# Performance work log

Hardware: AMD Instinct MI355X
Metric: run time of the kernel (lower is better)

## Reference

```python
import jax, jax.numpy as jnp
import numpy as np

N = 131072          # batch_size(64) * cycle_size(2048) total graph nodes
E = 2097152         # N * avg_degree(16) edges


def _gcn_block(x, edge_index, W_self, W_nbr, b):
    """GraphConv-style STGCN spatial block: self-transform + mean-aggregated
    neighbor transform over edge_index (gather -> segment-reduce -> scatter)."""
    src, dst = edge_index[0], edge_index[1]
    msg = jax.ops.segment_sum(x[src], dst, num_segments=N)            # [N, C_in]
    deg = jax.ops.segment_sum(jnp.ones((edge_index.shape[1],), x.dtype), dst,
                              num_segments=N)                          # [N]
    agg = msg / jnp.maximum(deg, 1.0)[:, None]
    return x @ W_self + agg @ W_nbr + b


def setup_inputs() -> dict:
    key = jax.random.key(0)
    ks = jax.random.split(key, 16)

    def lin(k, fan_in, fan_out):
        return jax.random.normal(k, (fan_in, fan_out), jnp.float32) / np.sqrt(fan_in)

    x = jax.random.normal(ks[0], (N, 16), jnp.float32)
    edge_index = jax.random.randint(ks[1], (2, E), 0, N)
    batch = jnp.zeros((N,), jnp.int64) if jax.config.jax_enable_x64 else jnp.zeros((N,), jnp.int32)

    return {
        "x": x,
        "edge_index": edge_index,
        "batch": batch,
        "W_lin": lin(ks[2], 16, 16),
        "b_lin": jnp.zeros((16,), jnp.float32),
        # block3: 16 -> 32
        "Ws3": lin(ks[3], 16, 32), "Wn3": lin(ks[4], 16, 32), "b3": jnp.zeros((32,), jnp.float32),
        # block2: 32 -> 64
        "Ws2": lin(ks[5], 32, 64), "Wn2": lin(ks[6], 32, 64), "b2": jnp.zeros((64,), jnp.float32),
        # block1: 64 -> 128
        "Ws1": lin(ks[7], 64, 128), "Wn1": lin(ks[8], 64, 128), "b1": jnp.zeros((128,), jnp.float32),
    }


def reference(x, edge_index, batch, W_lin, b_lin,
              Ws3, Wn3, b3, Ws2, Wn2, b2, Ws1, Wn1, b1):
    h = x @ W_lin + b_lin                                   # Linear(16,16)
    h = jax.nn.relu(_gcn_block(h, edge_index, Ws3, Wn3, b3))   # 16 -> 32
    h = jax.nn.relu(_gcn_block(h, edge_index, Ws2, Wn2, b2))   # 32 -> 64
    h = jax.nn.sigmoid(_gcn_block(h, edge_index, Ws1, Wn1, b1))  # 64 -> 128
    return h
```

## Files before the change

kernel.cpp:

```cpp
#include <hip/hip_runtime.h>
#include <cmath>


typedef __attribute__((ext_vector_type(8))) _Float16 half8;
typedef __attribute__((ext_vector_type(4))) float floatx4;

#define NBUCKET 512
#define BUCKET_SHIFT 8

__global__ __launch_bounds__(256) void bucket_hist_kernel(
    const int* __restrict__ dst, int* __restrict__ bcnt, int E, int EPB, int nblk) {
    __shared__ int lh[NBUCKET];
    for (int i = threadIdx.x; i < NBUCKET; i += 256) lh[i] = 0;
    __syncthreads();
    int base = blockIdx.x * EPB;
    int end  = min(base + EPB, E);
    for (int i = base + threadIdx.x; i < end; i += 256)
        atomicAdd(&lh[dst[i] >> BUCKET_SHIFT], 1);
    __syncthreads();
    for (int i = threadIdx.x; i < NBUCKET; i += 256)
        bcnt[i * nblk + blockIdx.x] = lh[i];
}

__global__ void scan1_kernel(const int* __restrict__ in, int* __restrict__ out,
                             int* __restrict__ bsum) {
    __shared__ int s[256];
    int i = blockIdx.x * 256 + threadIdx.x;
    int v = in[i];
    s[threadIdx.x] = v;
    __syncthreads();
    for (int off = 1; off < 256; off <<= 1) {
        int t = (threadIdx.x >= off) ? s[threadIdx.x - off] : 0;
        __syncthreads();
        s[threadIdx.x] += t;
        __syncthreads();
    }
    out[i] = s[threadIdx.x] - v;
    if (threadIdx.x == 255) bsum[blockIdx.x] = s[255];
}

__global__ void scan2_kernel(int* __restrict__ bsum, int NB) {
    extern __shared__ int s2[];
    int v = (threadIdx.x < NB) ? bsum[threadIdx.x] : 0;
    s2[threadIdx.x] = v;
    __syncthreads();
    for (int off = 1; off < NB; off <<= 1) {
        int t = (threadIdx.x >= off) ? s2[threadIdx.x - off] : 0;
        __syncthreads();
        s2[threadIdx.x] += t;
        __syncthreads();
    }
    if (threadIdx.x < NB) bsum[threadIdx.x] = s2[threadIdx.x] - v;
}

__global__ void scan3_kernel(int* __restrict__ out, const int* __restrict__ bsum) {
    int i = blockIdx.x * 256 + threadIdx.x;
    out[i] += bsum[blockIdx.x];
}

__global__ __launch_bounds__(256) void partition_kernel(
    const int* __restrict__ src, const int* __restrict__ dst,
    const int* __restrict__ bofs, int* __restrict__ part,
    int E, int EPB, int nblk) {
    __shared__ int cur[NBUCKET];
    for (int i = threadIdx.x; i < NBUCKET; i += 256)
        cur[i] = bofs[i * nblk + blockIdx.x];
    __syncthreads();
    int base = blockIdx.x * EPB;
    int end  = min(base + EPB, E);
    for (int i = base + threadIdx.x; i < end; i += 256) {
        int d = dst[i];
        int p = atomicAdd(&cur[d >> BUCKET_SHIFT], 1);
        part[p] = (src[i] << 8) | (d & 255);
    }
}

__global__ __launch_bounds__(256) void local_csr_kernel(
    const int* __restrict__ bofs, const int* __restrict__ part,
    int* __restrict__ row_ptr, int* __restrict__ csr_src,
    int N, int E, int nblk) {
    __shared__ int cnt[256];
    __shared__ int offs[256];
    const int u      = blockIdx.x;
    const int node0  = u << BUCKET_SHIFT;
    const int bstart = bofs[(size_t)u * nblk];
    const int bend   = (u + 1 < gridDim.x) ? bofs[(size_t)(u + 1) * nblk] : E;

    cnt[threadIdx.x] = 0;
    __syncthreads();
    for (int i = bstart + threadIdx.x; i < bend; i += 256)
        atomicAdd(&cnt[part[i] & 255], 1);
    __syncthreads();

    int v = cnt[threadIdx.x];
    offs[threadIdx.x] = v;
    __syncthreads();
    for (int off = 1; off < 256; off <<= 1) {
        int t = (threadIdx.x >= off) ? offs[threadIdx.x - off] : 0;
        __syncthreads();
        offs[threadIdx.x] += t;
        __syncthreads();
    }
    int excl = offs[threadIdx.x] - v;
    int rbase = bstart + excl;
    if (node0 + threadIdx.x < N) row_ptr[node0 + threadIdx.x] = rbase;
    if (u == 0 && threadIdx.x == 0) row_ptr[N] = E;
    __syncthreads();
    cnt[threadIdx.x] = rbase;
    __syncthreads();
    for (int i = bstart + threadIdx.x; i < bend; i += 256) {
        int e = part[i];
        int p = atomicAdd(&cnt[e & 255], 1);
        csr_src[p] = e >> 8;
    }
}

__global__ void wt_all_kernel(
    const float* __restrict__ Ws1, const float* __restrict__ Wn1, _Float16* __restrict__ Wt1,
    const float* __restrict__ Ws2, const float* __restrict__ Wn2, _Float16* __restrict__ Wt2,
    const float* __restrict__ Ws3, const float* __restrict__ Wn3, _Float16* __restrict__ Wt3) {
    int idx = blockIdx.x * 256 + threadIdx.x;
    const float *Ws, *Wn; _Float16* Wt; int CI, NOUT;
    if (idx < 16384)        { Ws = Ws1; Wn = Wn1; Wt = Wt1; CI = 64; NOUT = 128; }
    else if (idx < 20480)   { idx -= 16384; Ws = Ws2; Wn = Wn2; Wt = Wt2; CI = 32; NOUT = 64; }
    else if (idx < 21504)   { idx -= 20480; Ws = Ws3; Wn = Wn3; Wt = Wt3; CI = 16; NOUT = 32; }
    else return;
    int K = 2 * CI;
    int n = idx / K, k = idx - n * K;
    float v = (k < CI) ? Ws[(size_t)k * NOUT + n] : Wn[(size_t)(k - CI) * NOUT + n];
    Wt[n * K + k] = (_Float16)v;
}

__global__ void lin16_kernel(const float* __restrict__ x, const float* __restrict__ W,
                             const float* __restrict__ b, _Float16* __restrict__ h, int N) {
    __shared__ float sW[256];
    __shared__ float sb[16];
    sW[threadIdx.x] = W[threadIdx.x];
    if (threadIdx.x < 16) sb[threadIdx.x] = b[threadIdx.x];
    __syncthreads();
    int n = blockIdx.x * blockDim.x + threadIdx.x;
    if (n >= N) return;
    const float4* xr = (const float4*)(x + (size_t)n * 16);
    float4 x0 = xr[0], x1 = xr[1], x2 = xr[2], x3 = xr[3];
    float xi[16] = {x0.x, x0.y, x0.z, x0.w, x1.x, x1.y, x1.z, x1.w,
                    x2.x, x2.y, x2.z, x2.w, x3.x, x3.y, x3.z, x3.w};
    float o[16];
#pragma unroll
    for (int j = 0; j < 16; j++) o[j] = sb[j];
#pragma unroll
    for (int k = 0; k < 16; k++) {
        float xv = xi[k];
#pragma unroll
        for (int j = 0; j < 16; j++) o[j] += xv * sW[k * 16 + j];
    }
    half8 h0v, h1v;
#pragma unroll
    for (int j = 0; j < 8; j++) { h0v[j] = (_Float16)o[j]; h1v[j] = (_Float16)o[j + 8]; }
    half8* hr = (half8*)(h + (size_t)n * 16);
    hr[0] = h0v;
    hr[1] = h1v;
}

template <int C>
__global__ __launch_bounds__(256) void gather_kernel(
    const int* __restrict__ row_ptr, const int* __restrict__ csr_src,
    const _Float16* __restrict__ h, _Float16* __restrict__ agg, int N) {
    constexpr int GP = C / 8;
    int t = blockIdx.x * blockDim.x + threadIdx.x;
    int total = N * GP;
    if (t >= total) return;
    int n = t / GP;
    int g = t - n * GP;
    const int beg = row_ptr[n];
    const int end = row_ptr[n + 1];
    const size_t goff = (size_t)g * 8;

    float a0[8], a1[8];
#pragma unroll
    for (int i = 0; i < 8; i++) { a0[i] = 0.f; a1[i] = 0.f; }

    int j = beg;
    for (; j + 8 <= end; j += 8) {
        int i0 = csr_src[j + 0], i1 = csr_src[j + 1], i2 = csr_src[j + 2], i3 = csr_src[j + 3];
        int i4 = csr_src[j + 4], i5 = csr_src[j + 5], i6 = csr_src[j + 6], i7 = csr_src[j + 7];
        half8 v0 = *(const half8*)(h + (size_t)i0 * C + goff);
        half8 v1 = *(const half8*)(h + (size_t)i1 * C + goff);
        half8 v2 = *(const half8*)(h + (size_t)i2 * C + goff);
        half8 v3 = *(const half8*)(h + (size_t)i3 * C + goff);
        half8 v4 = *(const half8*)(h + (size_t)i4 * C + goff);
        half8 v5 = *(const half8*)(h + (size_t)i5 * C + goff);
        half8 v6 = *(const half8*)(h + (size_t)i6 * C + goff);
        half8 v7 = *(const half8*)(h + (size_t)i7 * C + goff);
#pragma unroll
        for (int i = 0; i < 8; i++) {
            a0[i] += ((float)v0[i] + (float)v2[i]) + ((float)v4[i] + (float)v6[i]);
            a1[i] += ((float)v1[i] + (float)v3[i]) + ((float)v5[i] + (float)v7[i]);
        }
    }
    if (j < end) {
        const int last = end - 1;
        int i0 = csr_src[j];
        int i1 = csr_src[min(j + 1, last)];
        int i2 = csr_src[min(j + 2, last)];
        int i3 = csr_src[min(j + 3, last)];
        int i4 = csr_src[min(j + 4, last)];
        int i5 = csr_src[min(j + 5, last)];
        int i6 = csr_src[min(j + 6, last)];
        int i7 = csr_src[min(j + 7, last)];
        half8 v0 = *(const half8*)(h + (size_t)i0 * C + goff);
        half8 v1 = *(const half8*)(h + (size_t)i1 * C + goff);
        half8 v2 = *(const half8*)(h + (size_t)i2 * C + goff);
        half8 v3 = *(const half8*)(h + (size_t)i3 * C + goff);
        half8 v4 = *(const half8*)(h + (size_t)i4 * C + goff);
        half8 v5 = *(const half8*)(h + (size_t)i5 * C + goff);
        half8 v6 = *(const half8*)(h + (size_t)i6 * C + goff);
        half8 v7 = *(const half8*)(h + (size_t)i7 * C + goff);
        float w1 = (j + 1 < end) ? 1.f : 0.f;
        float w2 = (j + 2 < end) ? 1.f : 0.f;
        float w3 = (j + 3 < end) ? 1.f : 0.f;
        float w4 = (j + 4 < end) ? 1.f : 0.f;
        float w5 = (j + 5 < end) ? 1.f : 0.f;
        float w6 = (j + 6 < end) ? 1.f : 0.f;
        float w7 = (j + 7 < end) ? 1.f : 0.f;
#pragma unroll
        for (int i = 0; i < 8; i++) {
            a0[i] += ((float)v0[i] + w2 * (float)v2[i]) + (w4 * (float)v4[i] + w6 * (float)v6[i]);
            a1[i] += (w1 * (float)v1[i] + w3 * (float)v3[i]) + (w5 * (float)v5[i] + w7 * (float)v7[i]);
        }
    }

    float inv = 1.0f / fmaxf((float)(end - beg), 1.0f);
    half8 r;
#pragma unroll
    for (int i = 0; i < 8; i++) r[i] = (_Float16)((a0[i] + a1[i]) * inv);
    *(half8*)(agg + (size_t)n * C + goff) = r;
}

template <int CI, int NOUT, int ACT, bool OUT_F16>
__global__ __launch_bounds__(256) void mfma_gemm_kernel(
    const _Float16* __restrict__ hbuf, const _Float16* __restrict__ abuf,
    const _Float16* __restrict__ Wt,
    const float* __restrict__ bias, void* __restrict__ outp, int N)
{
    constexpr int K   = 2 * CI;
    constexpr int KS  = K / 32;
    constexpr int CT  = NOUT / 16;
    constexpr int LDW = K + 8;
    __shared__ _Float16 Bt[NOUT * LDW];

    const int tid = threadIdx.x;
    for (int idx = tid; idx < NOUT * (K / 8); idx += 256) {
        int n  = idx / (K / 8);
        int kq = idx - n * (K / 8);
        *(half8*)&Bt[n * LDW + kq * 8] = *(const half8*)(Wt + (size_t)n * K + kq * 8);
    }
    __syncthreads();

    const int wave = tid >> 6;
    const int lane = tid & 63;
    const int m    = lane & 15;
    const int quad = lane >> 4;
    const int row0 = blockIdx.x * 64 + wave * 16;
    const size_t row = (size_t)(row0 + m);

    floatx4 acc[CT];
#pragma unroll
    for (int c = 0; c < CT; c++) acc[c] = (floatx4){0.f, 0.f, 0.f, 0.f};

#pragma unroll
    for (int s = 0; s < KS; s++) {
        int k8 = s * 32 + quad * 8;
        const _Float16* Ap = (k8 < CI) ? (hbuf + row * CI + k8)
                                       : (abuf + row * CI + (k8 - CI));
        half8 a = *(const half8*)Ap;
#pragma unroll
        for (int c = 0; c < CT; c++) {
            half8 b = *(const half8*)&Bt[(c * 16 + m) * LDW + k8];
            acc[c] = __builtin_amdgcn_mfma_f32_16x16x32_f16(a, b, acc[c], 0, 0, 0);
        }
    }

#pragma unroll
    for (int c = 0; c < CT; c++) {
        int col = c * 16 + m;
        float bv = bias[col];
#pragma unroll
        for (int j = 0; j < 4; j++) {
            int orow = row0 + quad * 4 + j;
            float v = acc[c][j] + bv;
            if (ACT == 0) v = fmaxf(v, 0.0f);
            else          v = 1.0f / (1.0f + __expf(-v));
            if (OUT_F16) ((_Float16*)outp)[(size_t)orow * NOUT + col] = (_Float16)v;
            else         ((float*)outp)[(size_t)orow * NOUT + col] = v;
        }
    }
}

extern "C" void kernel_launch(void* const* d_in, const int* in_sizes, int n_in,
                              void* d_out, int out_size, void* d_ws, size_t ws_size,
                              hipStream_t stream) {
    const float* x     = (const float*)d_in[0];
    const int*   ei    = (const int*)d_in[1];
    const float* W_lin = (const float*)d_in[3];
    const float* b_lin = (const float*)d_in[4];
    const float* Ws3   = (const float*)d_in[5];
    const float* Wn3   = (const float*)d_in[6];
    const float* b3    = (const float*)d_in[7];
    const float* Ws2   = (const float*)d_in[8];
    const float* Wn2   = (const float*)d_in[9];
    const float* b2    = (const float*)d_in[10];
    const float* Ws1   = (const float*)d_in[11];
    const float* Wn1   = (const float*)d_in[12];
    const float* b1    = (const float*)d_in[13];
    float* out = (float*)d_out;

    const int N = in_sizes[0] / 16;
    const int E = in_sizes[1] / 2;
    const int* src = ei;
    const int* dst = ei + E;

    const int NBLK = 256;
    const int EPB  = (E + NBLK - 1) / NBLK;
    const int M    = NBUCKET * NBLK;
    const int NB2  = M / 256;

    int* wsi = (int*)d_ws;
    int* row_ptr = wsi;
    size_t B0 = ((size_t)(N + 1) + 3) & ~(size_t)3;
    int* bcnt = wsi + B0;
    int* bofs = bcnt + M;
    int* bsum = bofs + M;
    size_t C0 = (B0 + 2 * (size_t)M + (size_t)NB2 + 3) & ~(size_t)3;
    int* csr_src = wsi + C0;
    size_t P0 = (C0 + (size_t)E + 3) & ~(size_t)3;
    int* part = wsi + P0;
    size_t H0 = (P0 + (size_t)E + 3) & ~(size_t)3;
    _Float16* regA = (_Float16*)(wsi + H0);
    _Float16* regB = regA + (size_t)64 * N;
    _Float16* Wt1  = regB + (size_t)64 * N;
    _Float16* Wt2  = Wt1 + 16384;
    _Float16* Wt3  = Wt2 + 4096;

    _Float16* h0    = regA;
    _Float16* agg16 = regA + (size_t)16 * N;
    _Float16* h2    = regA;
    _Float16* h3    = regB;
    _Float16* agg32 = regB + (size_t)32 * N;
    _Float16* agg64 = regB;

    const int BLK = 256;

    wt_all_kernel<<<(21504 + 255) / 256, 256, 0, stream>>>(
        Ws1, Wn1, Wt1, Ws2, Wn2, Wt2, Ws3, Wn3, Wt3);

    bucket_hist_kernel<<<NBLK, 256, 0, stream>>>(dst, bcnt, E, EPB, NBLK);
    scan1_kernel<<<NB2, 256, 0, stream>>>(bcnt, bofs, bsum);
    scan2_kernel<<<1, NB2, NB2 * sizeof(int), stream>>>(bsum, NB2);
    scan3_kernel<<<NB2, 256, 0, stream>>>(bofs, bsum);
    partition_kernel<<<NBLK, 256, 0, stream>>>(src, dst, bofs, part, E, EPB, NBLK);
    local_csr_kernel<<<NBUCKET, 256, 0, stream>>>(bofs, part, row_ptr, csr_src, N, E, NBLK);

    lin16_kernel<<<(N + BLK - 1) / BLK, BLK, 0, stream>>>(x, W_lin, b_lin, h0, N);

    gather_kernel<16><<<((size_t)N * 2 + BLK - 1) / BLK, BLK, 0, stream>>>(row_ptr, csr_src, h0, agg16, N);
    mfma_gemm_kernel<16, 32, 0, true><<<N / 64, 256, 0, stream>>>(h0, agg16, Wt3, b3, h3, N);

    gather_kernel<32><<<((size_t)N * 4 + BLK - 1) / BLK, BLK, 0, stream>>>(row_ptr, csr_src, h3, agg32, N);
    mfma_gemm_kernel<32, 64, 0, true><<<N / 64, 256, 0, stream>>>(h3, agg32, Wt2, b2, h2, N);

    gather_kernel<64><<<((size_t)N * 8 + BLK - 1) / BLK, BLK, 0, stream>>>(row_ptr, csr_src, h2, agg64, N);
    mfma_gemm_kernel<64, 128, 1, false><<<N / 64, 256, 0, stream>>>(h2, agg64, Wt1, b1, out, N);
}
```

Baseline: 325.0 us.

## Quantize post-ReLU activations to uint8 for the neighbor gathers

The GEMM now tracks the global maximum of each ReLU output with block-level and global atomicMax. A new kernel uses that maximum to quantize the fp16 activations to uint8, and new integer gather kernels accumulate the uint8 neighbor features and rescale them into fp16 means. The aim is to halve the bytes read in the random-access gathers for the 32- and 64-channel layers. In exchange it adds an extra quantize pass, an atomic reduction per block, and 8-bit quantization error in the aggregated features.

After: 346.2 us. +6.5%, slower.

```diff
diff --git a/kernel.cpp b/kernel.cpp
--- a/kernel.cpp
+++ b/kernel.cpp
@@ -7,6 +7,8 @@
 
 #define NBUCKET 512
 #define BUCKET_SHIFT 8
+
+__global__ void init_scales_kernel(int* __restrict__ g) { g[0] = 0; g[1] = 0; }
 
 __global__ __launch_bounds__(256) void bucket_hist_kernel(
     const int* __restrict__ dst, int* __restrict__ bcnt, int E, int EPB, int nblk) {
@@ -236,17 +238,121 @@
     *(half8*)(agg + (size_t)n * C + goff) = r;
 }
 
-template <int CI, int NOUT, int ACT, bool OUT_F16>
+__global__ __launch_bounds__(256) void quant_kernel(
+    const _Float16* __restrict__ h, const int* __restrict__ maxbits,
+    unsigned char* __restrict__ q, int total16) {
+    int t = blockIdx.x * 256 + threadIdx.x;
+    if (t >= total16) return;
+    float M = __int_as_float(*maxbits);
+    float inv = (M > 1e-20f) ? 255.0f / M : 0.0f;
+    const half8* hp = (const half8*)(h + (size_t)t * 16);
+    half8 v0 = hp[0], v1 = hp[1];
+    unsigned int dw[4] = {0u, 0u, 0u, 0u};
+#pragma unroll
+    for (int i = 0; i < 8; i++) {
+        unsigned int b = (unsigned int)((float)v0[i] * inv + 0.5f);
+        if (b > 255u) b = 255u;
+        dw[i >> 2] |= b << ((i & 3) * 8);
+    }
+#pragma unroll
+    for (int i = 0; i < 8; i++) {
+        unsigned int b = (unsigned int)((float)v1[i] * inv + 0.5f);
+        if (b > 255u) b = 255u;
+        dw[2 + (i >> 2)] |= b << ((i & 3) * 8);
+    }
+    uint4 o; o.x = dw[0]; o.y = dw[1]; o.z = dw[2]; o.w = dw[3];
+    *(uint4*)(q + (size_t)t * 16) = o;
+}
+
+#define ACC4(d, o)                                 \
+    { unsigned int _d = (d);                        \
+      a[(o)]     += _d & 0xffu;                     \
+      a[(o) + 1] += (_d >> 8) & 0xffu;              \
+      a[(o) + 2] += (_d >> 16) & 0xffu;             \
+      a[(o) + 3] += _d >> 24; }
+#define ACC4W(d, w, o)                              \
+    { unsigned int _d = (d); int _w = (w);          \
+      a[(o)]     += _w * (int)(_d & 0xffu);         \
+      a[(o) + 1] += _w * (int)((_d >> 8) & 0xffu);  \
+      a[(o) + 2] += _w * (int)((_d >> 16) & 0xffu); \
+      a[(o) + 3] += _w * (int)(_d >> 24); }
+
+template <int C>
+__global__ __launch_bounds__(256) void gatherq_kernel(
+    const int* __restrict__ row_ptr, const int* __restrict__ csr_src,
+    const unsigned char* __restrict__ hq, const int* __restrict__ maxbits,
+    _Float16* __restrict__ agg, int N) {
+    constexpr int GP = C / 16;
+    int t = blockIdx.x * 256 + threadIdx.x;
+    if (t >= N * GP) return;
+    int n = t / GP;
+    int g = t & (GP - 1);
+    const int beg = row_ptr[n];
+    const int end = row_ptr[n + 1];
+    const size_t goff = (size_t)g * 16;
+
+    int a[16];
+#pragma unroll
+    for (int i = 0; i < 16; i++) a[i] = 0;
+
+    int j = beg;
+    for (; j + 4 <= end; j += 4) {
+        int i0 = csr_src[j + 0], i1 = csr_src[j + 1];
+        int i2 = csr_src[j + 2], i3 = csr_src[j + 3];
+        uint4 q0 = *(const uint4*)(hq + (size_t)i0 * C + goff);
+        uint4 q1 = *(const uint4*)(hq + (size_t)i1 * C + goff);
+        uint4 q2 = *(const uint4*)(hq + (size_t)i2 * C + goff);
+        uint4 q3 = *(const uint4*)(hq + (size_t)i3 * C + goff);
+        ACC4(q0.x, 0) ACC4(q0.y, 4) ACC4(q0.z, 8) ACC4(q0.w, 12)
+        ACC4(q1.x, 0) ACC4(q1.y, 4) ACC4(q1.z, 8) ACC4(q1.w, 12)
+        ACC4(q2.x, 0) ACC4(q2.y, 4) ACC4(q2.z, 8) ACC4(q2.w, 12)
+        ACC4(q3.x, 0) ACC4(q3.y, 4) ACC4(q3.z, 8) ACC4(q3.w, 12)
+    }
+    if (j < end) {
+        const int last = end - 1;
+        int i0 = csr_src[j];
+        int i1 = csr_src[min(j + 1, last)];
+        int i2 = csr_src[min(j + 2, last)];
+        int i3 = csr_src[min(j + 3, last)];
+        uint4 q0 = *(const uint4*)(hq + (size_t)i0 * C + goff);
+        uint4 q1 = *(const uint4*)(hq + (size_t)i1 * C + goff);
+        uint4 q2 = *(const uint4*)(hq + (size_t)i2 * C + goff);
+        uint4 q3 = *(const uint4*)(hq + (size_t)i3 * C + goff);
+        int w1 = (j + 1 < end) ? 1 : 0;
+        int w2 = (j + 2 < end) ? 1 : 0;
+        int w3 = (j + 3 < end) ? 1 : 0;
+        ACC4(q0.x, 0) ACC4(q0.y, 4) ACC4(q0.z, 8) ACC4(q0.w, 12)
+        ACC4W(q1.x, w1, 0) ACC4W(q1.y, w1, 4) ACC4W(q1.z, w1, 8) ACC4W(q1.w, w1, 12)
+        ACC4W(q2.x, w2, 0) ACC4W(q2.y, w2, 4) ACC4W(q2.z, w2, 8) ACC4W(q2.w, w2, 12)
+        ACC4W(q3.x, w3, 0) ACC4W(q3.y, w3, 4) ACC4W(q3.z, w3, 8) ACC4W(q3.w, w3, 12)
+    }
+
+    float M = __int_as_float(*maxbits);
+    float sc = (M * (1.0f / 255.0f)) / fmaxf((float)(end - beg), 1.0f);
+    half8 rl, rh;
+#pragma unroll
+    for (int i = 0; i < 8; i++) {
+        rl[i] = (_Float16)((float)a[i] * sc);
+        rh[i] = (_Float16)((float)a[i + 8] * sc);
+    }
+    half8* ap = (half8*)(agg + (size_t)n * C + goff);
+    ap[0] = rl;
+    ap[1] = rh;
+}
+
+template <int CI, int NOUT, int ACT, bool OUT_F16, bool TRACKMAX>
 __global__ __launch_bounds__(256) void mfma_gemm_kernel(
     const _Float16* __restrict__ hbuf, const _Float16* __restrict__ abuf,
     const _Float16* __restrict__ Wt,
-    const float* __restrict__ bias, void* __restrict__ outp, int N)
+    const float* __restrict__ bias, void* __restrict__ outp,
+    int* __restrict__ maxbits, int N)
 {
     constexpr int K   = 2 * CI;
     constexpr int KS  = K / 32;
     constexpr int CT  = NOUT / 16;
     constexpr int LDW = K + 8;
     __shared__ _Float16 Bt[NOUT * LDW];
+    __shared__ int smax;
 
     const int tid = threadIdx.x;
     for (int idx = tid; idx < NOUT * (K / 8); idx += 256) {
@@ -254,6 +360,7 @@
         int kq = idx - n * (K / 8);
         *(half8*)&Bt[n * LDW + kq * 8] = *(const half8*)(Wt + (size_t)n * K + kq * 8);
     }
+    if (TRACKMAX && tid == 0) smax = 0;
     __syncthreads();
 
     const int wave = tid >> 6;
@@ -280,6 +387,7 @@
         }
     }
 
+    float tmax = 0.0f;
 #pragma unroll
     for (int c = 0; c < CT; c++) {
         int col = c * 16 + m;
@@ -290,9 +398,15 @@
             float v = acc[c][j] + bv;
             if (ACT == 0) v = fmaxf(v, 0.0f);
             else          v = 1.0f / (1.0f + __expf(-v));
+            if (TRACKMAX) tmax = fmaxf(tmax, v);
             if (OUT_F16) ((_Float16*)outp)[(size_t)orow * NOUT + col] = (_Float16)v;
             else         ((float*)outp)[(size_t)orow * NOUT + col] = v;
         }
+    }
+    if (TRACKMAX) {
+        atomicMax(&smax, __float_as_int(tmax));
+        __syncthreads();
+        if (tid == 0) atomicMax(maxbits, smax);
     }
 }
 
@@ -330,11 +444,12 @@
     int* bcnt = wsi + B0;
     int* bofs = bcnt + M;
     int* bsum = bofs + M;
-    size_t C0 = (B0 + 2 * (size_t)M + (size_t)NB2 + 3) & ~(size_t)3;
+    int* gmax = bsum + NB2;
+    size_t C0 = (B0 + 2 * (size_t)M + (size_t)NB2 + 2 + 3) & ~(size_t)3;
     int* csr_src = wsi + C0;
     size_t P0 = (C0 + (size_t)E + 3) & ~(size_t)3;
     int* part = wsi + P0;
-    size_t H0 = (P0 + (size_t)E + 3) & ~(size_t)3;
+    size_t H0 = (P0 + 2 * (size_t)E + 3) & ~(size_t)3;
     _Float16* regA = (_Float16*)(wsi + H0);
     _Float16* regB = regA + (size_t)64 * N;
     _Float16* Wt1  = regB + (size_t)64 * N;
@@ -348,7 +463,12 @@
     _Float16* agg32 = regB + (size_t)32 * N;
     _Float16* agg64 = regB;
 
+    unsigned char* h3q = (unsigned char*)part;
+    unsigned char* h2q = (unsigned char*)part + (size_t)32 * N;
+
     const int BLK = 256;
+
+    init_scales_kernel<<<1, 1, 0, stream>>>(gmax);
 
     wt_all_kernel<<<(21504 + 255) / 256, 256, 0, stream>>>(
         Ws1, Wn1, Wt1, Ws2, Wn2, Wt2, Ws3, Wn3, Wt3);
@@ -363,11 +483,18 @@
     lin16_kernel<<<(N + BLK - 1) / BLK, BLK, 0, stream>>>(x, W_lin, b_lin, h0, N);
 
     gather_kernel<16><<<((size_t)N * 2 + BLK - 1) / BLK, BLK, 0, stream>>>(row_ptr, csr_src, h0, agg16, N);
-    mfma_gemm_kernel<16, 32, 0, true><<<N / 64, 256, 0, stream>>>(h0, agg16, Wt3, b3, h3, N);
-
-    gather_kernel<32><<<((size_t)N * 4 + BLK - 1) / BLK, BLK, 0, stream>>>(row_ptr, csr_src, h3, agg32, N);
-    mfma_gemm_kernel<32, 64, 0, true><<<N / 64, 256, 0, stream>>>(h3, agg32, Wt2, b2, h2, N);
-
-    gather_kernel<64><<<((size_t)N * 8 + BLK - 1) / BLK, BLK, 0, stream>>>(row_ptr, csr_src, h2, agg64, N);
-    mfma_gemm_kernel<64, 128, 1, false><<<N / 64, 256, 0, stream>>>(h2, agg64, Wt1, b1, out, N);
-}
+    mfma_gemm_kernel<16, 32, 0, true, true><<<N / 64, 256, 0, stream>>>(
+        h0, agg16, Wt3, b3, h3, gmax + 0, N);
+
+    quant_kernel<<<(N * 2 + BLK - 1) / BLK, BLK, 0, stream>>>(h3, gmax + 0, h3q, N * 2);
+    gatherq_kernel<32><<<((size_t)N * 2 + BLK - 1) / BLK, BLK, 0, stream>>>(
+        row_ptr, csr_src, h3q, gmax + 0, agg32, N);
+    mfma_gemm_kernel<32, 64, 0, true, true><<<N / 64, 256, 0, stream>>>(
+        h3, agg32, Wt2, b2, h2, gmax + 1, N);
+
+    quant_kernel<<<(N * 4 + BLK - 1) / BLK, BLK, 0, stream>>>(h2, gmax + 1, h2q, N * 4);
+    gatherq_kernel<64><<<((size_t)N * 4 + BLK - 1) / BLK, BLK, 0, stream>>>(
+        row_ptr, csr_src, h2q, gmax + 1, agg64, N);
+    mfma_gemm_kernel<64, 128, 1, false, false><<<N / 64, 256, 0, stream>>>(
+        h2, agg64, Wt1, b1, out, nullptr, N);
+}
```
